# Kernel optimization log

Hardware: AMD Instinct MI355X
Metric: run time of the kernel (lower is better)

## Reference

```python
import jax, jax.numpy as jnp
import numpy as np

K_HOPS = 3
NUM_GRAPHS = 64
GN_EPS = 1e-5


def setup_inputs() -> dict:
    key = jax.random.key(0)
    ks = jax.random.split(key, 6)
    N, E, F = 50000, 625000, 128
    y = jax.random.normal(ks[0], (N, F), dtype=jnp.float32)
    edge_index = jax.random.randint(ks[1], (2, E), 0, N, dtype=jnp.int64)
    edge_weight = jax.random.uniform(ks[2], (E,), dtype=jnp.float32)
    batch = jnp.sort(jax.random.randint(ks[3], (N,), 0, NUM_GRAPHS, dtype=jnp.int64))
    tag_w = jax.random.normal(ks[4], (K_HOPS + 1, F, F), dtype=jnp.float32) * (1.0 / np.sqrt(F))
    tag_b = jnp.zeros((F,), dtype=jnp.float32)
    gn_weight = jnp.ones((F,), dtype=jnp.float32)
    gn_bias = jnp.zeros((F,), dtype=jnp.float32)
    gn_mean_scale = jnp.ones((F,), dtype=jnp.float32)
    return {"y": y, "edge_index": edge_index, "edge_weight": edge_weight,
            "batch": batch, "tag_w": tag_w, "tag_b": tag_b,
            "gn_weight": gn_weight, "gn_bias": gn_bias, "gn_mean_scale": gn_mean_scale}


def reference(y, edge_index, edge_weight, batch, tag_w, tag_b, gn_weight, gn_bias, gn_mean_scale):
    N = y.shape[0]
    src, dst = edge_index[0], edge_index[1]

    # --- TAGConv: symmetric gcn_norm (no self-loops), K hops ---
    deg = jax.ops.segment_sum(edge_weight, dst, num_segments=N)  # [N]
    dinv = jnp.where(deg > 0, jax.lax.rsqrt(jnp.maximum(deg, 1e-30)), 0.0)
    norm = dinv[src] * edge_weight * dinv[dst]  # [E]

    h = y
    out = h @ tag_w[0]
    for k in range(1, K_HOPS + 1):
        # one hop of message passing: gather from src, scatter-sum at dst
        h = jax.ops.segment_sum(norm[:, None] * h[src], dst, num_segments=N)  # [N,F]
        out = out + h @ tag_w[k]
    out = out + tag_b

    # --- GraphNorm over per-graph segments ---
    cnt = jax.ops.segment_sum(jnp.ones((N,), out.dtype), batch, num_segments=NUM_GRAPHS)
    cnt = jnp.maximum(cnt, 1.0)[:, None]  # [G,1]
    mean = jax.ops.segment_sum(out, batch, num_segments=NUM_GRAPHS) / cnt  # [G,F]
    xc = out - gn_mean_scale * mean[batch]
    var = jax.ops.segment_sum(xc * xc, batch, num_segments=NUM_GRAPHS) / cnt  # [G,F]
    hn = gn_weight * xc * jax.lax.rsqrt(var[batch] + GN_EPS) + gn_bias

    # --- activation; dropout is identity in eval mode; residual ---
    h_act = jax.nn.relu(hn)
    return y + h_act
```

## Files before the change

### kernel.cpp

```cpp
#include <hip/hip_runtime.h>

#define F 128
#define GRAPHS 64
#define GN_EPS 1e-5f
#define SCAN_B 256

typedef short short8 __attribute__((ext_vector_type(8)));
typedef float f32x4 __attribute__((ext_vector_type(4)));

__device__ __forceinline__ unsigned short f2b(float f) {
    unsigned u = __float_as_uint(f);
    unsigned r = (u + 0x7fffu + ((u >> 16) & 1u)) >> 16;
    return (unsigned short)r;
}
__device__ __forceinline__ float b2f(unsigned short h) {
    return __uint_as_float(((unsigned)h) << 16);
}

__global__ void prep_kernel(const int* __restrict__ ei, const float* __restrict__ ew,
                            unsigned long long* __restrict__ packed,
                            unsigned short* __restrict__ rank, int E, int ebl,
                            const float4* __restrict__ y, ushort4* __restrict__ hs0,
                            int n4, int fbl,
                            const float* __restrict__ tw, unsigned short* __restrict__ wf) {
    int b = blockIdx.x;
    if (b < ebl) {
        int e = b * 256 + threadIdx.x;
        if (e < E) {
            int dst = ei[E + e];
            unsigned q = (unsigned)(ew[e] * 16777216.0f + 0.5f);
            unsigned long long old =
                atomicAdd(&packed[dst], (1ull << 40) | (unsigned long long)q);
            rank[e] = (unsigned short)(old >> 40);
        }
    } else if (b < ebl + fbl) {
        int i = (b - ebl) * 256 + threadIdx.x;
        if (i < n4) {
            float4 v = y[i];
            hs0[i] = make_ushort4(f2b(v.x), f2b(v.y), f2b(v.z), f2b(v.w));
        }
    } else {
        int i = (b - ebl - fbl) * 256 + threadIdx.x;
        int seg = i >> 14;
        int r = i & 16383;
        int kb = r >> 12;
        int wc = (r >> 11) & 1;
        int nt = (r >> 9) & 3;
        int lane = (r >> 3) & 63;
        int j = i & 7;
        int k = kb * 32 + (lane >> 4) * 8 + j;
        int n = wc * 64 + nt * 16 + (lane & 15);
        wf[i] = f2b(tw[seg * 16384 + k * 128 + n]);
    }
}

__global__ void node_prep_kernel(const unsigned long long* __restrict__ packed,
                                 float* __restrict__ dinv, const int* __restrict__ batch,
                                 int* __restrict__ gstart, int* __restrict__ excl,
                                 int* __restrict__ blockSums, int n) {
    __shared__ int s[SCAN_B];
    int i = blockIdx.x * SCAN_B + threadIdx.x;
    int v = 0;
    if (i < n) {
        unsigned long long p = packed[i];
        v = (int)(p >> 40);
        float d = (float)(p & 0xFFFFFFFFFFull) * 5.9604644775390625e-8f;
        dinv[i] = (d > 0.f) ? rsqrtf(fmaxf(d, 1e-30f)) : 0.f;
        int b = batch[i];
        if (i == 0) {
            for (int g = 0; g <= b; ++g) gstart[g] = 0;
        } else {
            int bp = batch[i - 1];
            for (int g = bp + 1; g <= b; ++g) gstart[g] = i;
        }
        if (i == n - 1) {
            for (int g = b + 1; g <= GRAPHS; ++g) gstart[g] = n;
        }
    }
    s[threadIdx.x] = v;
    __syncthreads();
    for (int off = 1; off < SCAN_B; off <<= 1) {
        int t = (threadIdx.x >= off) ? s[threadIdx.x - off] : 0;
        __syncthreads();
        s[threadIdx.x] += t;
        __syncthreads();
    }
    if (i < n) excl[i] = s[threadIdx.x] - v;
    if (threadIdx.x == SCAN_B - 1) blockSums[blockIdx.x] = s[SCAN_B - 1];
}

__global__ void scan3_kernel(int* __restrict__ offs, const int* __restrict__ blockSums,
                             int n, int total, int nb) {
    __shared__ int s[SCAN_B];
    int t = threadIdx.x;
    int v = (t < nb) ? blockSums[t] : 0;
    s[t] = v;
    __syncthreads();
    for (int off = 1; off < SCAN_B; off <<= 1) {
        int x = (t >= off) ? s[t - off] : 0;
        __syncthreads();
        s[t] += x;
        __syncthreads();
    }
    int pre = (blockIdx.x == 0) ? 0 : s[blockIdx.x - 1];
    int i = blockIdx.x * SCAN_B + t;
    if (i < n) offs[i] += pre;
    if (i == 0) offs[n] = total;
}

__global__ void scatter_kernel(const int* __restrict__ ei, const float* __restrict__ w,
                               const float* __restrict__ dinv, const int* __restrict__ offs,
                               const unsigned short* __restrict__ rank,
                               unsigned* __restrict__ csr, int E) {
    int e = blockIdx.x * blockDim.x + threadIdx.x;
    if (e >= E) return;
    int s = ei[e];
    int d = ei[E + e];
    unsigned v = ((unsigned)s << 16) | (unsigned)f2b(dinv[s] * w[e]);
    csr[offs[d] + (int)rank[e]] = v;
}

__global__ __launch_bounds__(256) void hop_kernel(const unsigned short* __restrict__ hin,
                                                  unsigned short* __restrict__ hout,
                                                  const int* __restrict__ offs,
                                                  const unsigned* __restrict__ csr,
                                                  const float* __restrict__ dinv, int n) {
    int lane = threadIdx.x & 63;
    int node = blockIdx.x * 4 + (threadIdx.x >> 6);
    if (node >= n) return;
    int g = lane >> 4, fl = lane & 15;
    int e0 = offs[node], e1 = offs[node + 1];
    float acc[8] = {};
    for (int j = e0; j < e1; j += 16) {
        int base = j + g * 4;
        int c0 = min(base + 0, e1 - 1), c1 = min(base + 1, e1 - 1);
        int c2 = min(base + 2, e1 - 1), c3 = min(base + 3, e1 - 1);
        unsigned ed0 = csr[c0], ed1 = csr[c1], ed2 = csr[c2], ed3 = csr[c3];
        float w0 = (base + 0 < e1) ? b2f((unsigned short)(ed0 & 0xffffu)) : 0.f;
        float w1 = (base + 1 < e1) ? b2f((unsigned short)(ed1 & 0xffffu)) : 0.f;
        float w2 = (base + 2 < e1) ? b2f((unsigned short)(ed2 & 0xffffu)) : 0.f;
        float w3 = (base + 3 < e1) ? b2f((unsigned short)(ed3 & 0xffffu)) : 0.f;
        short8 h0 = *(const short8*)(hin + (size_t)(ed0 >> 16) * 128 + fl * 8);
        short8 h1 = *(const short8*)(hin + (size_t)(ed1 >> 16) * 128 + fl * 8);
        short8 h2 = *(const short8*)(hin + (size_t)(ed2 >> 16) * 128 + fl * 8);
        short8 h3 = *(const short8*)(hin + (size_t)(ed3 >> 16) * 128 + fl * 8);
        #pragma unroll
        for (int k = 0; k < 8; ++k) {
            acc[k] += w0 * b2f((unsigned short)h0[k]) + w1 * b2f((unsigned short)h1[k]);
            acc[k] += w2 * b2f((unsigned short)h2[k]) + w3 * b2f((unsigned short)h3[k]);
        }
    }
    #pragma unroll
    for (int k = 0; k < 8; ++k) {
        acc[k] += __shfl_xor(acc[k], 16);
        acc[k] += __shfl_xor(acc[k], 32);
    }
    if (lane < 16) {
        float dd = dinv[node];
        short8 o;
        #pragma unroll
        for (int k = 0; k < 8; ++k) o[k] = (short)f2b(acc[k] * dd);
        *(short8*)(hout + (size_t)node * 128 + fl * 8) = o;
    }
}

__global__ __launch_bounds__(256) void gemm_kernel(const unsigned short* __restrict__ hcat,
                                                   const unsigned short* __restrict__ Wf,
                                                   const float* __restrict__ bias,
                                                   unsigned short* __restrict__ outb,
                                                   int M, size_t NF) {
    __shared__ unsigned short As[4][4096];
    int lane = threadIdx.x & 63;
    int wid = threadIdx.x >> 6;
    int wr = wid & 1, wc = wid >> 1;
    int quad = lane >> 4, l15 = lane & 15;
    int row0 = blockIdx.x * 64;
    unsigned short* myA = As[wid];
    f32x4 acc[2][4] = {};

    for (int s = 0; s < 4; ++s) {
        const unsigned short* Aseg = hcat + (size_t)s * NF;
        short8 stg[8];
        #pragma unroll
        for (int i = 0; i < 8; ++i) {
            int flat = i * 64 + lane;
            int r = flat >> 4, c = flat & 15;
            stg[i] = *(const short8*)(Aseg + (size_t)(row0 + wr * 32 + r) * 128 + c * 8);
        }
        #pragma unroll
        for (int i = 0; i < 8; ++i) {
            int flat = i * 64 + lane;
            int r = flat >> 4, c = flat & 15;
            *(short8*)&myA[(r * 16 + (c ^ (r & 15))) * 8] = stg[i];
        }
        #pragma unroll
        for (int kb = 0; kb < 4; ++kb) {
            int swz = ((kb * 4 + quad) ^ l15) * 8;
            short8 a0 = *(short8*)&myA[l15 * 128 + swz];
            short8 a1 = *(short8*)&myA[(16 + l15) * 128 + swz];
            const unsigned short* bb = Wf + (size_t)(((s * 4 + kb) * 2 + wc) * 4) * 512 + lane * 8;
            short8 b0 = *(const short8*)(bb + 0 * 512);
            short8 b1 = *(const short8*)(bb + 1 * 512);
            short8 b2 = *(const short8*)(bb + 2 * 512);
            short8 b3 = *(const short8*)(bb + 3 * 512);
            acc[0][0] = __builtin_amdgcn_mfma_f32_16x16x32_bf16(a0, b0, acc[0][0], 0, 0, 0);
            acc[0][1] = __builtin_amdgcn_mfma_f32_16x16x32_bf16(a0, b1, acc[0][1], 0, 0, 0);
            acc[0][2] = __builtin_amdgcn_mfma_f32_16x16x32_bf16(a0, b2, acc[0][2], 0, 0, 0);
            acc[0][3] = __builtin_amdgcn_mfma_f32_16x16x32_bf16(a0, b3, acc[0][3], 0, 0, 0);
            acc[1][0] = __builtin_amdgcn_mfma_f32_16x16x32_bf16(a1, b0, acc[1][0], 0, 0, 0);
            acc[1][1] = __builtin_amdgcn_mfma_f32_16x16x32_bf16(a1, b1, acc[1][1], 0, 0, 0);
            acc[1][2] = __builtin_amdgcn_mfma_f32_16x16x32_bf16(a1, b2, acc[1][2], 0, 0, 0);
            acc[1][3] = __builtin_amdgcn_mfma_f32_16x16x32_bf16(a1, b3, acc[1][3], 0, 0, 0);
        }
    }

    #pragma unroll
    for (int mt = 0; mt < 2; ++mt) {
        #pragma unroll
        for (int r = 0; r < 4; ++r) {
            int row = row0 + wr * 32 + mt * 16 + quad * 4 + r;
            if (row < M) {
                #pragma unroll
                for (int nt = 0; nt < 4; ++nt) {
                    int col = wc * 64 + nt * 16 + l15;
                    outb[(size_t)row * 128 + col] = f2b(acc[mt][nt][r] + bias[col]);
                }
            }
        }
    }
}

#define STAT_NODES 32
__global__ __launch_bounds__(256) void stats_kernel(const unsigned* __restrict__ ob2,
                                                    const int* __restrict__ batch,
                                                    float* __restrict__ S1, float* __restrict__ S2,
                                                    int n) {
    int fp = threadIdx.x & 63;
    int par = threadIdx.x >> 6;
    int base = blockIdx.x * STAT_NODES;
    int n1 = min(base + STAT_NODES, n);
    int i0 = base + par;
    if (i0 >= n1) return;
    float s1a = 0.f, s2a = 0.f, s1b = 0.f, s2b = 0.f;
    int curg = batch[i0];
    for (int i = i0; i < n1; i += 4) {
        int g = batch[i];
        if (g != curg) {
            atomicAdd(&S1[curg * F + fp * 2 + 0], s1a);
            atomicAdd(&S2[curg * F + fp * 2 + 0], s2a);
            atomicAdd(&S1[curg * F + fp * 2 + 1], s1b);
            atomicAdd(&S2[curg * F + fp * 2 + 1], s2b);
            s1a = s2a = s1b = s2b = 0.f; curg = g;
        }
        unsigned v2 = ob2[(size_t)i * 64 + fp];
        float va = b2f((unsigned short)(v2 & 0xffffu));
        float vb = b2f((unsigned short)(v2 >> 16));
        s1a += va; s2a += va * va;
        s1b += vb; s2b += vb * vb;
    }
    atomicAdd(&S1[curg * F + fp * 2 + 0], s1a);
    atomicAdd(&S2[curg * F + fp * 2 + 0], s2a);
    atomicAdd(&S1[curg * F + fp * 2 + 1], s1b);
    atomicAdd(&S2[curg * F + fp * 2 + 1], s2b);
}

__global__ void final_kernel(const ushort4* __restrict__ yb, const ushort4* __restrict__ ob,
                             const int* __restrict__ batch, const float* __restrict__ S1,
                             const float* __restrict__ S2, const int* __restrict__ gstart,
                             const float* __restrict__ gnw, const float* __restrict__ gnb,
                             const float* __restrict__ gms,
                             float4* __restrict__ res, int n) {
    int idx = blockIdx.x * blockDim.x + threadIdx.x;
    if (idx >= n * 32) return;
    int node = idx >> 5;
    int q = idx & 31;
    int g = batch[node];
    float rc = 1.f / fmaxf((float)(gstart[g + 1] - gstart[g]), 1.f);
    int base = g * 128 + q * 4;
    float4 s1 = *(const float4*)&S1[base];
    float4 s2 = *(const float4*)&S2[base];
    float4 w  = *(const float4*)&gnw[q * 4];
    float4 bb = *(const float4*)&gnb[q * 4];
    float4 sc = *(const float4*)&gms[q * 4];
    ushort4 yv = yb[idx];
    ushort4 ov = ob[idx];
    float4 r;
    {
        float m = s1.x * rc, e2 = s2.x * rc, s = sc.x;
        float var = e2 - (2.f * s - s * s) * m * m;
        float A = w.x * rsqrtf(var + GN_EPS);
        r.x = b2f(yv.x) + fmaxf(0.f, (b2f(ov.x) - s * m) * A + bb.x);
    }
    {
        float m = s1.y * rc, e2 = s2.y * rc, s = sc.y;
        float var = e2 - (2.f * s - s * s) * m * m;
        float A = w.y * rsqrtf(var + GN_EPS);
        r.y = b2f(yv.y) + fmaxf(0.f, (b2f(ov.y) - s * m) * A + bb.y);
    }
    {
        float m = s1.z * rc, e2 = s2.z * rc, s = sc.z;
        float var = e2 - (2.f * s - s * s) * m * m;
        float A = w.z * rsqrtf(var + GN_EPS);
        r.z = b2f(yv.z) + fmaxf(0.f, (b2f(ov.z) - s * m) * A + bb.z);
    }
    {
        float m = s1.w * rc, e2 = s2.w * rc, s = sc.w;
        float var = e2 - (2.f * s - s * s) * m * m;
        float A = w.w * rsqrtf(var + GN_EPS);
        r.w = b2f(yv.w) + fmaxf(0.f, (b2f(ov.w) - s * m) * A + bb.w);
    }
    res[idx] = r;
}

extern "C" void kernel_launch(void* const* d_in, const int* in_sizes, int n_in,
                              void* d_out, int out_size, void* d_ws, size_t ws_size,
                              hipStream_t stream) {
    const float* y     = (const float*)d_in[0];
    const int*   ei    = (const int*)d_in[1];
    const float* ew    = (const float*)d_in[2];
    const int*   batch = (const int*)d_in[3];
    const float* tag_w = (const float*)d_in[4];
    const float* tag_b = (const float*)d_in[5];
    const float* gnw   = (const float*)d_in[6];
    const float* gnb   = (const float*)d_in[7];
    const float* gms   = (const float*)d_in[8];
    float* res = (float*)d_out;

    const int N = in_sizes[0] / F;
    const int E = in_sizes[1] / 2;
    const size_t NF = (size_t)N * F;

    char* p = (char*)d_ws;
    unsigned long long* packed = (unsigned long long*)p; p += (size_t)N * 8;
    float* S1 = (float*)p;       p += (size_t)GRAPHS * F * 4;
    float* S2 = (float*)p;       p += (size_t)GRAPHS * F * 4;
    size_t zeroBytes = (size_t)(p - (char*)d_ws);
    int*   gstart = (int*)p;     p += 512;
    float* dinv = (float*)p;     p += (size_t)N * 4;
    int*   offs = (int*)p;       p += (size_t)(N + 4) * 4;
    int*   blockSums = (int*)p;  p += 4096;
    unsigned short* rank = (unsigned short*)p; p += ((size_t)E * 2 + 15) & ~15ull;
    unsigned* csr = (unsigned*)p; p += (size_t)E * 4;
    unsigned short* Wf = (unsigned short*)p; p += 4 * 128 * 128 * 2;
    unsigned short* hcat = (unsigned short*)p; p += NF * 2 * 4;
    unsigned short* outb = (unsigned short*)p; p += NF * 2;
    p += 4096;

    hipMemsetAsync(d_ws, 0, zeroBytes, stream);

    int eb = (E + 255) / 256;
    int sb = (N + SCAN_B - 1) / SCAN_B;
    int n4 = N * 32;
    int fb = (n4 + 255) / 256;
    int wb = (4 * 128 * 128) / 256;

    unsigned short* hs0 = hcat;
    unsigned short* hs1 = hcat + NF;
    unsigned short* hs2 = hcat + 2 * NF;
    unsigned short* hs3 = hcat + 3 * NF;

    prep_kernel<<<eb + fb + wb, 256, 0, stream>>>(ei, ew, packed, rank, E, eb,
                                                  (const float4*)y, (ushort4*)hs0, n4, fb,
                                                  tag_w, Wf);
    node_prep_kernel<<<sb, SCAN_B, 0, stream>>>(packed, dinv, batch, gstart, offs, blockSums, N);
    scan3_kernel<<<sb, SCAN_B, 0, stream>>>(offs, blockSums, N, E, sb);
    scatter_kernel<<<eb, 256, 0, stream>>>(ei, ew, dinv, offs, rank, csr, E);

    int hb = (N + 3) / 4;
    hop_kernel<<<hb, 256, 0, stream>>>(hs0, hs1, offs, csr, dinv, N);
    hop_kernel<<<hb, 256, 0, stream>>>(hs1, hs2, offs, csr, dinv, N);
    hop_kernel<<<hb, 256, 0, stream>>>(hs2, hs3, offs, csr, dinv, N);

    gemm_kernel<<<(N + 63) / 64, 256, 0, stream>>>(hcat, Wf, tag_b, outb, N, NF);

    stats_kernel<<<(N + STAT_NODES - 1) / STAT_NODES, 256, 0, stream>>>((const unsigned*)outb,
                                                                        batch, S1, S2, N);

    final_kernel<<<(N * 32 + 255) / 256, 256, 0, stream>>>((const ushort4*)hs0, (const ushort4*)outb,
                                                           batch, S1, S2, gstart, gnw, gnb, gms,
                                                           (float4*)res, N);
}
```

Baseline: 261.6 us.

## Build CSR via two-level bucket partition instead of global 64-bit atomics

Replaces the global per-node atomic counting (packed degree and count, with a rank per edge) with a radix-style build. Per-block shared-memory histograms over 256-node buckets are scanned, edges are partitioned into buckets, and each bucket block computes degrees, offsets and CSR slots in shared memory. A final pass folds dinv[src] into the stored weights. The goal is to cut contended global atomics and scattered writes, at the cost of more kernel launches and an extra E*8-byte intermediate pass. The edge order inside each CSR row is now nondeterministic, and the weight is rounded to bf16 twice.

After: 248.0 us. 1.06x faster.

```diff
diff --git a/kernel.cpp b/kernel.cpp
--- a/kernel.cpp
+++ b/kernel.cpp
@@ -4,6 +4,7 @@
 #define GRAPHS 64
 #define GN_EPS 1e-5f
 #define SCAN_B 256
+#define PB 256
 
 typedef short short8 __attribute__((ext_vector_type(8)));
 typedef float f32x4 __attribute__((ext_vector_type(4)));
@@ -17,30 +18,31 @@
     return __uint_as_float(((unsigned)h) << 16);
 }
 
-__global__ void prep_kernel(const int* __restrict__ ei, const float* __restrict__ ew,
-                            unsigned long long* __restrict__ packed,
-                            unsigned short* __restrict__ rank, int E, int ebl,
+__global__ __launch_bounds__(256) void prep_kernel(const int* __restrict__ ei,
+                            int* __restrict__ hist_t, int E, int NB, int chunk,
                             const float4* __restrict__ y, ushort4* __restrict__ hs0,
                             int n4, int fbl,
-                            const float* __restrict__ tw, unsigned short* __restrict__ wf) {
+                            const float* __restrict__ tw, unsigned short* __restrict__ wf,
+                            const int* __restrict__ batch, int* __restrict__ gstart, int n) {
     int b = blockIdx.x;
-    if (b < ebl) {
-        int e = b * 256 + threadIdx.x;
-        if (e < E) {
-            int dst = ei[E + e];
-            unsigned q = (unsigned)(ew[e] * 16777216.0f + 0.5f);
-            unsigned long long old =
-                atomicAdd(&packed[dst], (1ull << 40) | (unsigned long long)q);
-            rank[e] = (unsigned short)(old >> 40);
-        }
-    } else if (b < ebl + fbl) {
-        int i = (b - ebl) * 256 + threadIdx.x;
+    if (b < PB) {
+        __shared__ int hist[256];
+        hist[threadIdx.x] = 0;
+        __syncthreads();
+        int e0 = b * chunk, e1 = min(e0 + chunk, E);
+        for (int e = e0 + threadIdx.x; e < e1; e += 256)
+            atomicAdd(&hist[ei[E + e] >> 8], 1);
+        __syncthreads();
+        for (int k = threadIdx.x; k < NB; k += 256)
+            hist_t[k * PB + b] = hist[k];
+    } else if (b < PB + fbl) {
+        int i = (b - PB) * 256 + threadIdx.x;
         if (i < n4) {
             float4 v = y[i];
             hs0[i] = make_ushort4(f2b(v.x), f2b(v.y), f2b(v.z), f2b(v.w));
         }
-    } else {
-        int i = (b - ebl - fbl) * 256 + threadIdx.x;
+    } else if (b < PB + fbl + 256) {
+        int i = (b - PB - fbl) * 256 + threadIdx.x;
         int seg = i >> 14;
         int r = i & 16383;
         int kb = r >> 12;
@@ -49,34 +51,30 @@
         int lane = (r >> 3) & 63;
         int j = i & 7;
         int k = kb * 32 + (lane >> 4) * 8 + j;
-        int n = wc * 64 + nt * 16 + (lane & 15);
-        wf[i] = f2b(tw[seg * 16384 + k * 128 + n]);
-    }
-}
-
-__global__ void node_prep_kernel(const unsigned long long* __restrict__ packed,
-                                 float* __restrict__ dinv, const int* __restrict__ batch,
-                                 int* __restrict__ gstart, int* __restrict__ excl,
-                                 int* __restrict__ blockSums, int n) {
+        int nn = wc * 64 + nt * 16 + (lane & 15);
+        wf[i] = f2b(tw[seg * 16384 + k * 128 + nn]);
+    } else {
+        int i = (b - PB - fbl - 256) * 256 + threadIdx.x;
+        if (i < n) {
+            int bb = batch[i];
+            if (i == 0) {
+                for (int g = 0; g <= bb; ++g) gstart[g] = 0;
+            } else {
+                int bp = batch[i - 1];
+                for (int g = bp + 1; g <= bb; ++g) gstart[g] = i;
+            }
+            if (i == n - 1) {
+                for (int g = bb + 1; g <= GRAPHS; ++g) gstart[g] = n;
+            }
+        }
+    }
+}
+
+__global__ void scanA_kernel(const int* __restrict__ in, int* __restrict__ ex,
+                             int* __restrict__ blockSums, int n) {
     __shared__ int s[SCAN_B];
     int i = blockIdx.x * SCAN_B + threadIdx.x;
-    int v = 0;
-    if (i < n) {
-        unsigned long long p = packed[i];
-        v = (int)(p >> 40);
-        float d = (float)(p & 0xFFFFFFFFFFull) * 5.9604644775390625e-8f;
-        dinv[i] = (d > 0.f) ? rsqrtf(fmaxf(d, 1e-30f)) : 0.f;
-        int b = batch[i];
-        if (i == 0) {
-            for (int g = 0; g <= b; ++g) gstart[g] = 0;
-        } else {
-            int bp = batch[i - 1];
-            for (int g = bp + 1; g <= b; ++g) gstart[g] = i;
-        }
-        if (i == n - 1) {
-            for (int g = b + 1; g <= GRAPHS; ++g) gstart[g] = n;
-        }
-    }
+    int v = (i < n) ? in[i] : 0;
     s[threadIdx.x] = v;
     __syncthreads();
     for (int off = 1; off < SCAN_B; off <<= 1) {
@@ -85,12 +83,12 @@
         s[threadIdx.x] += t;
         __syncthreads();
     }
-    if (i < n) excl[i] = s[threadIdx.x] - v;
+    if (i < n) ex[i] = s[threadIdx.x] - v;
     if (threadIdx.x == SCAN_B - 1) blockSums[blockIdx.x] = s[SCAN_B - 1];
 }
 
-__global__ void scan3_kernel(int* __restrict__ offs, const int* __restrict__ blockSums,
-                             int n, int total, int nb) {
+__global__ void scanB_kernel(int* __restrict__ ex, const int* __restrict__ blockSums,
+                             int n, int nb) {
     __shared__ int s[SCAN_B];
     int t = threadIdx.x;
     int v = (t < nb) ? blockSums[t] : 0;
@@ -104,20 +102,86 @@
     }
     int pre = (blockIdx.x == 0) ? 0 : s[blockIdx.x - 1];
     int i = blockIdx.x * SCAN_B + t;
-    if (i < n) offs[i] += pre;
-    if (i == 0) offs[n] = total;
-}
-
-__global__ void scatter_kernel(const int* __restrict__ ei, const float* __restrict__ w,
-                               const float* __restrict__ dinv, const int* __restrict__ offs,
-                               const unsigned short* __restrict__ rank,
-                               unsigned* __restrict__ csr, int E) {
-    int e = blockIdx.x * blockDim.x + threadIdx.x;
-    if (e >= E) return;
-    int s = ei[e];
-    int d = ei[E + e];
-    unsigned v = ((unsigned)s << 16) | (unsigned)f2b(dinv[s] * w[e]);
-    csr[offs[d] + (int)rank[e]] = v;
+    if (i < n) ex[i] += pre;
+}
+
+__global__ __launch_bounds__(256) void part_kernel(const int* __restrict__ ei,
+                                                   const float* __restrict__ ew,
+                                                   const int* __restrict__ ex,
+                                                   uint2* __restrict__ part,
+                                                   int E, int NB, int chunk) {
+    __shared__ int cur[256];
+    int k = blockIdx.x;
+    for (int b = threadIdx.x; b < NB; b += 256) cur[b] = ex[b * PB + k];
+    __syncthreads();
+    int e0 = k * chunk, e1 = min(e0 + chunk, E);
+    for (int e = e0 + threadIdx.x; e < e1; e += 256) {
+        int dst = ei[E + e];
+        int src = ei[e];
+        float w = ew[e];
+        int slot = atomicAdd(&cur[dst >> 8], 1);
+        part[slot] = make_uint2(((unsigned)dst << 16) | (unsigned)src, __float_as_uint(w));
+    }
+}
+
+__global__ __launch_bounds__(256) void bucket_kernel(const uint2* __restrict__ part,
+                                                     const int* __restrict__ ex,
+                                                     float* __restrict__ dinv,
+                                                     int* __restrict__ offs,
+                                                     unsigned* __restrict__ csr,
+                                                     int N, int NB, int E) {
+    __shared__ float degf[256];
+    __shared__ int cnte[256];
+    __shared__ int scn[256];
+    __shared__ int cur2[256];
+    int b = blockIdx.x, t = threadIdx.x;
+    degf[t] = 0.f;
+    cnte[t] = 0;
+    __syncthreads();
+    int s0 = ex[b * PB];
+    int s1 = (b + 1 < NB) ? ex[(b + 1) * PB] : E;
+    for (int i = s0 + t; i < s1; i += 256) {
+        uint2 p = part[i];
+        int dl = (p.x >> 16) & 255;
+        atomicAdd(&degf[dl], __uint_as_float(p.y));
+        atomicAdd(&cnte[dl], 1);
+    }
+    __syncthreads();
+    int v = cnte[t];
+    scn[t] = v;
+    __syncthreads();
+    for (int off = 1; off < 256; off <<= 1) {
+        int x = (t >= off) ? scn[t - off] : 0;
+        __syncthreads();
+        scn[t] += x;
+        __syncthreads();
+    }
+    int node = b * 256 + t;
+    int base = s0 + scn[t] - v;
+    if (node < N) {
+        float d = degf[t];
+        dinv[node] = (d > 0.f) ? rsqrtf(fmaxf(d, 1e-30f)) : 0.f;
+        offs[node] = base;
+    }
+    if (b == 0 && t == 0) offs[N] = E;
+    cur2[t] = base;
+    __syncthreads();
+    for (int i = s0 + t; i < s1; i += 256) {
+        uint2 p = part[i];
+        int dl = (p.x >> 16) & 255;
+        unsigned src = p.x & 0xffffu;
+        int slot = atomicAdd(&cur2[dl], 1);
+        csr[slot] = (src << 16) | (unsigned)f2b(__uint_as_float(p.y));
+    }
+}
+
+__global__ void wfix_kernel(unsigned* __restrict__ csr, const float* __restrict__ dinv, int E) {
+    int i = blockIdx.x * 256 + threadIdx.x;
+    if (i >= E) return;
+    unsigned v = csr[i];
+    unsigned src = v >> 16;
+    float w = b2f((unsigned short)(v & 0xffffu)) * dinv[src];
+    csr[i] = (src << 16) | (unsigned)f2b(w);
 }
 
 __global__ __launch_bounds__(256) void hop_kernel(const unsigned short* __restrict__ hin,
@@ -329,17 +393,21 @@
     const int N = in_sizes[0] / F;
     const int E = in_sizes[1] / 2;
     const size_t NF = (size_t)N * F;
+    const int NB = (N + 255) >> 8;
+    const int NH = NB * PB;
+    const int chunk = (E + PB - 1) / PB;
 
     char* p = (char*)d_ws;
-    unsigned long long* packed = (unsigned long long*)p; p += (size_t)N * 8;
     float* S1 = (float*)p;       p += (size_t)GRAPHS * F * 4;
     float* S2 = (float*)p;       p += (size_t)GRAPHS * F * 4;
     size_t zeroBytes = (size_t)(p - (char*)d_ws);
     int*   gstart = (int*)p;     p += 512;
     float* dinv = (float*)p;     p += (size_t)N * 4;
     int*   offs = (int*)p;       p += (size_t)(N + 4) * 4;
+    int*   hist_t = (int*)p;     p += (size_t)NH * 4;
+    int*   ex = (int*)p;         p += (size_t)(NH + 4) * 4;
     int*   blockSums = (int*)p;  p += 4096;
-    unsigned short* rank = (unsigned short*)p; p += ((size_t)E * 2 + 15) & ~15ull;
+    uint2* part = (uint2*)p;     p += (size_t)E * 8;
     unsigned* csr = (unsigned*)p; p += (size_t)E * 4;
     unsigned short* Wf = (unsigned short*)p; p += 4 * 128 * 128 * 2;
     unsigned short* hcat = (unsigned short*)p; p += NF * 2 * 4;
@@ -348,23 +416,24 @@
 
     hipMemsetAsync(d_ws, 0, zeroBytes, stream);
 
-    int eb = (E + 255) / 256;
-    int sb = (N + SCAN_B - 1) / SCAN_B;
     int n4 = N * 32;
     int fb = (n4 + 255) / 256;
-    int wb = (4 * 128 * 128) / 256;
+    int gb = (N + 255) / 256;
+    int hsb = (NH + SCAN_B - 1) / SCAN_B;
 
     unsigned short* hs0 = hcat;
     unsigned short* hs1 = hcat + NF;
     unsigned short* hs2 = hcat + 2 * NF;
     unsigned short* hs3 = hcat + 3 * NF;
 
-    prep_kernel<<<eb + fb + wb, 256, 0, stream>>>(ei, ew, packed, rank, E, eb,
-                                                  (const float4*)y, (ushort4*)hs0, n4, fb,
-                                                  tag_w, Wf);
-    node_prep_kernel<<<sb, SCAN_B, 0, stream>>>(packed, dinv, batch, gstart, offs, blockSums, N);
-    scan3_kernel<<<sb, SCAN_B, 0, stream>>>(offs, blockSums, N, E, sb);
-    scatter_kernel<<<eb, 256, 0, stream>>>(ei, ew, dinv, offs, rank, csr, E);
+    prep_kernel<<<PB + fb + 256 + gb, 256, 0, stream>>>(ei, hist_t, E, NB, chunk,
+                                                        (const float4*)y, (ushort4*)hs0, n4, fb,
+                                                        tag_w, Wf, batch, gstart, N);
+    scanA_kernel<<<hsb, SCAN_B, 0, stream>>>(hist_t, ex, blockSums, NH);
+    scanB_kernel<<<hsb, SCAN_B, 0, stream>>>(ex, blockSums, NH, hsb);
+    part_kernel<<<PB, 256, 0, stream>>>(ei, ew, ex, part, E, NB, chunk);
+    bucket_kernel<<<NB, 256, 0, stream>>>(part, ex, dinv, offs, csr, N, NB, E);
+    wfix_kernel<<<(E + 255) / 256, 256, 0, stream>>>(csr, dinv, E);
 
     int hb = (N + 3) / 4;
     hop_kernel<<<hb, 256, 0, stream>>>(hs0, hs1, offs, csr, dinv, N);
```
